# Optimization experiments

Measured on AMD Instinct MI355X. Metric: run time of the kernel, lower is better.

Reference implementation:

```python
import jax, jax.numpy as jnp
import numpy as np

N_NODES = 50000
N_EDGES = 800000
D_IN, D_HID, D_OUT = 128, 128, 64
BN_EPS = 1e-5


def gcn_conv(x, W, b, src, dst, ew, n):
    # PyG GCNConv: out[i] = sum_j norm_ij * (x @ W)[j] + b, with self-loops added
    xw = x @ W                                   # [N, D_out]
    loop = jnp.arange(n)
    s = jnp.concatenate([src, loop])             # add self-loops (weight 1)
    d = jnp.concatenate([dst, loop])
    w = jnp.concatenate([ew, jnp.ones((n,), x.dtype)])
    deg = jax.ops.segment_sum(w, d, num_segments=n)
    dinv = jnp.where(deg > 0, jax.lax.rsqrt(deg), 0.0)
    norm = dinv[s] * w * dinv[d]                 # symmetric normalization
    msg = xw[s] * norm[:, None]                  # gather + scale  [E+N, D_out]
    return jax.ops.segment_sum(msg, d, num_segments=n) + b


def setup_inputs() -> dict:
    key = jax.random.key(0)
    ks = jax.random.split(key, 12)
    x = jax.random.normal(ks[0], (N_NODES, D_IN), dtype=jnp.float32)
    edge_index = jax.random.randint(ks[1], (2, N_EDGES), 0, N_NODES, dtype=jnp.int64)
    edge_weight = jax.random.uniform(ks[2], (N_EDGES,), dtype=jnp.float32)
    W1 = jax.random.normal(ks[3], (D_IN, D_HID), dtype=jnp.float32) * 0.05
    b1 = jnp.zeros((D_HID,), jnp.float32)
    gamma = jnp.ones((D_HID,), jnp.float32)
    beta = jnp.zeros((D_HID,), jnp.float32)
    running_mean = jax.random.normal(ks[4], (D_HID,), dtype=jnp.float32) * 0.1
    running_var = jax.random.uniform(ks[5], (D_HID,), dtype=jnp.float32) + 0.5
    W2 = jax.random.normal(ks[6], (D_HID, D_OUT), dtype=jnp.float32) * 0.05
    b2 = jnp.zeros((D_OUT,), jnp.float32)
    return {"x": x, "edge_index": edge_index, "edge_weight": edge_weight,
            "W1": W1, "b1": b1, "gamma": gamma, "beta": beta,
            "running_mean": running_mean, "running_var": running_var,
            "W2": W2, "b2": b2}


def reference(x, edge_index, edge_weight, W1, b1, gamma, beta,
              running_mean, running_var, W2, b2):
    src, dst = edge_index[0], edge_index[1]
    n = x.shape[0]
    h = gcn_conv(x, W1, b1, src, dst, edge_weight, n)
    # BatchNorm1d in eval mode (running stats); dropout inactive in eval
    h = (h - running_mean) * jax.lax.rsqrt(running_var + BN_EPS) * gamma + beta
    h = jax.nn.relu(h)
    out = gcn_conv(h, W2, b2, src, dst, edge_weight, n)
    return out
```

## Files before the change

### kernel.cpp

```cpp
#include <hip/hip_runtime.h>
#include <hip/hip_fp16.h>

#define BN_EPS 1e-5f
#define PAD 64

typedef __attribute__((ext_vector_type(8))) short short8;
typedef __attribute__((ext_vector_type(4))) float f32x4;

static __device__ __forceinline__ unsigned short f2bf(float f) {
    unsigned u = __float_as_uint(f);
    u += 0x7FFF + ((u >> 16) & 1);
    return (unsigned short)(u >> 16);
}
static __device__ __forceinline__ float bf2f(unsigned short b) {
    return __uint_as_float((unsigned)b << 16);
}
static __device__ __forceinline__ unsigned pk(int s, float w) {
    return ((unsigned)s << 16) | (unsigned)__half_as_ushort(__float2half_rn(w));
}
static __device__ __forceinline__ float pw(unsigned e) {
    return __half2float(__ushort_as_half((unsigned short)(e & 0xFFFFu)));
}

__global__ __launch_bounds__(256) void k_fused(const int* __restrict__ src, const int* __restrict__ dst,
                                               const float* __restrict__ ew,
                                               int* cnt, unsigned* __restrict__ pad, int e, int gfill, int stride,
                                               const float* __restrict__ A, const float* __restrict__ W,
                                               unsigned short* __restrict__ C, int n,
                                               const float* __restrict__ b1, const float* __restrict__ gamma,
                                               const float* __restrict__ beta, const float* __restrict__ mean,
                                               const float* __restrict__ var,
                                               float* __restrict__ bnscale, float* __restrict__ bnshift,
                                               const float* __restrict__ W2, unsigned short* __restrict__ w2bf) {
    __shared__ unsigned short W1s[16384];
    int tid = threadIdx.x;
    int b = (int)blockIdx.x;
    int gGemm = (n + 63) / 64;

    bool isFill = ((b % stride) == 0) && (b / stride < gfill);
    if (isFill) {
        int i0 = ((b / stride) * 256 + tid) * 8;
        if (i0 + 7 < e) {
            int4   s0 = *(const int4*)(src + i0), s1 = *(const int4*)(src + i0 + 4);
            int4   d0 = *(const int4*)(dst + i0), d1 = *(const int4*)(dst + i0 + 4);
            float4 w0 = *(const float4*)(ew + i0), w1 = *(const float4*)(ew + i0 + 4);
            int p0 = atomicAdd(&cnt[d0.x], 1);
            int p1 = atomicAdd(&cnt[d0.y], 1);
            int p2 = atomicAdd(&cnt[d0.z], 1);
            int p3 = atomicAdd(&cnt[d0.w], 1);
            int p4 = atomicAdd(&cnt[d1.x], 1);
            int p5 = atomicAdd(&cnt[d1.y], 1);
            int p6 = atomicAdd(&cnt[d1.z], 1);
            int p7 = atomicAdd(&cnt[d1.w], 1);
            if (p0 < PAD) pad[(size_t)d0.x * PAD + p0] = pk(s0.x, w0.x);
            if (p1 < PAD) pad[(size_t)d0.y * PAD + p1] = pk(s0.y, w0.y);
            if (p2 < PAD) pad[(size_t)d0.z * PAD + p2] = pk(s0.z, w0.z);
            if (p3 < PAD) pad[(size_t)d0.w * PAD + p3] = pk(s0.w, w0.w);
            if (p4 < PAD) pad[(size_t)d1.x * PAD + p4] = pk(s1.x, w1.x);
            if (p5 < PAD) pad[(size_t)d1.y * PAD + p5] = pk(s1.y, w1.y);
            if (p6 < PAD) pad[(size_t)d1.z * PAD + p6] = pk(s1.z, w1.z);
            if (p7 < PAD) pad[(size_t)d1.w * PAD + p7] = pk(s1.w, w1.w);
        } else {
            for (int i = i0; i < e; ++i) {
                int d = dst[i];
                int p = atomicAdd(&cnt[d], 1);
                if (p < PAD) pad[(size_t)d * PAD + p] = pk(src[i], ew[i]);
            }
        }
        return;
    }

    int fillsBefore = (b == 0) ? 0 : min(gfill, (b - 1) / stride + 1);
    int g = b - fillsBefore;
    if (g == gGemm) {
        if (tid < 128) {
            float sc = gamma[tid] * rsqrtf(var[tid] + BN_EPS);
            bnscale[tid] = sc;
            bnshift[tid] = (b1[tid] - mean[tid]) * sc + beta[tid];
        }
        const float4* W4 = (const float4*)W2;
        ushort4* O = (ushort4*)w2bf;
        #pragma unroll
        for (int q = 0; q < 8; ++q) {
            float4 v = W4[q * 256 + tid];
            O[q * 256 + tid] = make_ushort4(f2bf(v.x), f2bf(v.y), f2bf(v.z), f2bf(v.w));
        }
        return;
    }

    int row0 = g * 64;

    {
        int k  = tid >> 1;
        int c0 = (tid & 1) * 64;
        int kk = k >> 5, lg = (k >> 3) & 3, ii = k & 7;
        int tbase = kk * 4096 + lg * 128 + ii;
        const float4* Wr = (const float4*)(W + (size_t)k * 128 + c0);
        #pragma unroll
        for (int j = 0; j < 16; ++j) {
            float4 v = Wr[j];
            int n0 = c0 + j * 4;
            W1s[tbase + ((n0 + 0) >> 4) * 512 + ((n0 + 0) & 15) * 8] = f2bf(v.x);
            W1s[tbase + ((n0 + 1) >> 4) * 512 + ((n0 + 1) & 15) * 8] = f2bf(v.y);
            W1s[tbase + ((n0 + 2) >> 4) * 512 + ((n0 + 2) & 15) * 8] = f2bf(v.z);
            W1s[tbase + ((n0 + 3) >> 4) * 512 + ((n0 + 3) & 15) * 8] = f2bf(v.w);
        }
    }
    __syncthreads();

    int w = tid >> 6, lane = tid & 63;
    int arow = row0 + w * 16 + (lane & 15);
    if (arow > n - 1) arow = n - 1;
    const float* xrow = A + (size_t)arow * 128 + ((lane >> 4) * 8);
    const unsigned short* Wl = W1s + (size_t)lane * 8;

    f32x4 z = {0.f, 0.f, 0.f, 0.f};
    f32x4 acc0 = z, acc1 = z, acc2 = z, acc3 = z, acc4 = z, acc5 = z, acc6 = z, acc7 = z;

    #pragma unroll
    for (int kk = 0; kk < 4; ++kk) {
        float4 v0 = *(const float4*)(xrow + kk * 32);
        float4 v1 = *(const float4*)(xrow + kk * 32 + 4);
        short8 a;
        a[0] = (short)f2bf(v0.x); a[1] = (short)f2bf(v0.y);
        a[2] = (short)f2bf(v0.z); a[3] = (short)f2bf(v0.w);
        a[4] = (short)f2bf(v1.x); a[5] = (short)f2bf(v1.y);
        a[6] = (short)f2bf(v1.z); a[7] = (short)f2bf(v1.w);
        const unsigned short* Wk = Wl + kk * 4096;
        short8 b0 = *(const short8*)(Wk);
        short8 b1 = *(const short8*)(Wk + 512);
        short8 b2 = *(const short8*)(Wk + 1024);
        short8 b3 = *(const short8*)(Wk + 1536);
        short8 b4 = *(const short8*)(Wk + 2048);
        short8 b5 = *(const short8*)(Wk + 2560);
        short8 b6 = *(const short8*)(Wk + 3072);
        short8 b7 = *(const short8*)(Wk + 3584);
        acc0 = __builtin_amdgcn_mfma_f32_16x16x32_bf16(a, b0, acc0, 0, 0, 0);
        acc1 = __builtin_amdgcn_mfma_f32_16x16x32_bf16(a, b1, acc1, 0, 0, 0);
        acc2 = __builtin_amdgcn_mfma_f32_16x16x32_bf16(a, b2, acc2, 0, 0, 0);
        acc3 = __builtin_amdgcn_mfma_f32_16x16x32_bf16(a, b3, acc3, 0, 0, 0);
        acc4 = __builtin_amdgcn_mfma_f32_16x16x32_bf16(a, b4, acc4, 0, 0, 0);
        acc5 = __builtin_amdgcn_mfma_f32_16x16x32_bf16(a, b5, acc5, 0, 0, 0);
        acc6 = __builtin_amdgcn_mfma_f32_16x16x32_bf16(a, b6, acc6, 0, 0, 0);
        acc7 = __builtin_amdgcn_mfma_f32_16x16x32_bf16(a, b7, acc7, 0, 0, 0);
    }

    int rw = row0 + w * 16 + ((lane >> 4) << 2);
    int cb = lane & 15;
    #define STORE_NT(av, nt)                                                              \
        if (rw + 0 < n) C[(size_t)(rw + 0) * 128 + (nt)*16 + cb] = f2bf(av[0]);           \
        if (rw + 1 < n) C[(size_t)(rw + 1) * 128 + (nt)*16 + cb] = f2bf(av[1]);           \
        if (rw + 2 < n) C[(size_t)(rw + 2) * 128 + (nt)*16 + cb] = f2bf(av[2]);           \
        if (rw + 3 < n) C[(size_t)(rw + 3) * 128 + (nt)*16 + cb] = f2bf(av[3]);
    STORE_NT(acc0, 0) STORE_NT(acc1, 1) STORE_NT(acc2, 2) STORE_NT(acc3, 3)
    STORE_NT(acc4, 4) STORE_NT(acc5, 5) STORE_NT(acc6, 6) STORE_NT(acc7, 7)
    #undef STORE_NT
}

__global__ __launch_bounds__(256) void k_deg(const int* __restrict__ cnt, const unsigned* __restrict__ pad,
                                             float* __restrict__ dinv, int n) {
    int i = blockIdx.x * 256 + threadIdx.x;
    if (i < n) {
        int c = min(cnt[i], PAD);
        size_t base = (size_t)i * PAD;
        const uint4* row = (const uint4*)(pad + base);
        float s = 1.0f;
        int p = 0;
        for (; p + 3 < c; p += 4) {
            uint4 v = row[p >> 2];
            s += pw(v.x) + pw(v.y) + pw(v.z) + pw(v.w);
        }
        for (; p < c; ++p) s += pw(pad[base + p]);
        dinv[i] = rsqrtf(s);
    }
}

__global__ __launch_bounds__(256) void k_ag12(const unsigned short* __restrict__ xw, const int* __restrict__ cnt,
                                              const unsigned* __restrict__ pad,
                                              const float* __restrict__ dinv,
                                              const float* __restrict__ scale, const float* __restrict__ shift,
                                              const unsigned short* __restrict__ w2bf,
                                              unsigned short* __restrict__ hw2, int n) {
    __shared__ unsigned short W2s[128 * 64];
    int tid = threadIdx.x;
    {
        const uint4* s4 = (const uint4*)w2bf;
        uint4* d4 = (uint4*)W2s;
        #pragma unroll
        for (int q = 0; q < 4; ++q) d4[q * 256 + tid] = s4[q * 256 + tid];
    }
    __syncthreads();

    int g = tid >> 5;
    int lc = tid & 31;
    int node = blockIdx.x * 8 + g;
    if (node >= n) return;

    unsigned hu0, hu1;
    {
        const ushort4* X4 = (const ushort4*)xw;
        float di = dinv[node];
        int c = min(cnt[node], PAD);
        size_t base = (size_t)node * PAD;
        ushort4 q0 = X4[(size_t)node * 32 + lc];
        float4 acc0 = make_float4(bf2f(q0.x) * di, bf2f(q0.y) * di, bf2f(q0.z) * di, bf2f(q0.w) * di);
        float4 acc1 = make_float4(0, 0, 0, 0);
        float4 acc2 = make_float4(0, 0, 0, 0);
        float4 acc3 = make_float4(0, 0, 0, 0);
        int p = 0;
        for (; p + 3 < c; p += 4) {
            uint4 ee = *(const uint4*)(pad + base + p);
            float w0 = pw(ee.x) * dinv[ee.x >> 16];
            float w1 = pw(ee.y) * dinv[ee.y >> 16];
            float w2 = pw(ee.z) * dinv[ee.z >> 16];
            float w3 = pw(ee.w) * dinv[ee.w >> 16];
            ushort4 a = X4[(size_t)(ee.x >> 16) * 32 + lc];
            ushort4 b = X4[(size_t)(ee.y >> 16) * 32 + lc];
            ushort4 gg = X4[(size_t)(ee.z >> 16) * 32 + lc];
            ushort4 d = X4[(size_t)(ee.w >> 16) * 32 + lc];
            acc0.x += w0 * bf2f(a.x); acc0.y += w0 * bf2f(a.y); acc0.z += w0 * bf2f(a.z); acc0.w += w0 * bf2f(a.w);
            acc1.x += w1 * bf2f(b.x); acc1.y += w1 * bf2f(b.y); acc1.z += w1 * bf2f(b.z); acc1.w += w1 * bf2f(b.w);
            acc2.x += w2 * bf2f(gg.x); acc2.y += w2 * bf2f(gg.y); acc2.z += w2 * bf2f(gg.z); acc2.w += w2 * bf2f(gg.w);
            acc3.x += w3 * bf2f(d.x); acc3.y += w3 * bf2f(d.y); acc3.z += w3 * bf2f(d.z); acc3.w += w3 * bf2f(d.w);
        }
        for (; p < c; ++p) {
            unsigned e0 = pad[base + p];
            float w0 = pw(e0) * dinv[e0 >> 16];
            ushort4 a = X4[(size_t)(e0 >> 16) * 32 + lc];
            acc0.x += w0 * bf2f(a.x); acc0.y += w0 * bf2f(a.y); acc0.z += w0 * bf2f(a.z); acc0.w += w0 * bf2f(a.w);
        }
        acc0.x = (acc0.x + acc1.x + acc2.x + acc3.x) * di;
        acc0.y = (acc0.y + acc1.y + acc2.y + acc3.y) * di;
        acc0.z = (acc0.z + acc1.z + acc2.z + acc3.z) * di;
        acc0.w = (acc0.w + acc1.w + acc2.w + acc3.w) * di;
        float4 Sc = ((const float4*)scale)[lc];
        float4 Sh = ((const float4*)shift)[lc];
        unsigned short r0 = f2bf(fmaxf(acc0.x * Sc.x + Sh.x, 0.0f));
        unsigned short r1 = f2bf(fmaxf(acc0.y * Sc.y + Sh.y, 0.0f));
        unsigned short r2 = f2bf(fmaxf(acc0.z * Sc.z + Sh.z, 0.0f));
        unsigned short r3 = f2bf(fmaxf(acc0.w * Sc.w + Sh.w, 0.0f));
        hu0 = ((unsigned)r1 << 16) | (unsigned)r0;
        hu1 = ((unsigned)r3 << 16) | (unsigned)r2;
    }

    float a0 = 0.0f, a1 = 0.0f;
    const unsigned* W2u = (const unsigned*)W2s;
    #pragma unroll 8
    for (int k = 0; k < 32; ++k) {
        unsigned p0 = (unsigned)__shfl((int)hu0, k, 32);
        unsigned p1 = (unsigned)__shfl((int)hu1, k, 32);
        float h0 = bf2f((unsigned short)(p0 & 0xFFFFu));
        float h1 = bf2f((unsigned short)(p0 >> 16));
        float h2 = bf2f((unsigned short)(p1 & 0xFFFFu));
        float h3 = bf2f((unsigned short)(p1 >> 16));
        unsigned w0u = W2u[(4 * k + 0) * 32 + lc];
        unsigned w1u = W2u[(4 * k + 1) * 32 + lc];
        unsigned w2u = W2u[(4 * k + 2) * 32 + lc];
        unsigned w3u = W2u[(4 * k + 3) * 32 + lc];
        a0 += h0 * bf2f((unsigned short)(w0u & 0xFFFFu));
        a1 += h0 * bf2f((unsigned short)(w0u >> 16));
        a0 += h1 * bf2f((unsigned short)(w1u & 0xFFFFu));
        a1 += h1 * bf2f((unsigned short)(w1u >> 16));
        a0 += h2 * bf2f((unsigned short)(w2u & 0xFFFFu));
        a1 += h2 * bf2f((unsigned short)(w2u >> 16));
        a0 += h3 * bf2f((unsigned short)(w3u & 0xFFFFu));
        a1 += h3 * bf2f((unsigned short)(w3u >> 16));
    }
    unsigned outp = ((unsigned)f2bf(a1) << 16) | (unsigned)f2bf(a0);
    ((unsigned*)hw2)[(size_t)node * 32 + lc] = outp;
}

__global__ __launch_bounds__(256) void k_agg2(const unsigned short* __restrict__ hw, const int* __restrict__ cnt,
                                              const unsigned* __restrict__ pad,
                                              const float* __restrict__ dinv,
                                              const float* __restrict__ b2, float* __restrict__ out, int n) {
    int node = blockIdx.x * 16 + (threadIdx.x >> 4);
    if (node >= n) return;
    int lc = threadIdx.x & 15;
    const ushort4* X4 = (const ushort4*)hw;
    float di = dinv[node];
    int c = min(cnt[node], PAD);
    size_t base = (size_t)node * PAD;
    ushort4 q0 = X4[(size_t)node * 16 + lc];
    float4 acc0 = make_float4(bf2f(q0.x) * di, bf2f(q0.y) * di, bf2f(q0.z) * di, bf2f(q0.w) * di);
    float4 acc1 = make_float4(0, 0, 0, 0);
    float4 acc2 = make_float4(0, 0, 0, 0);
    float4 acc3 = make_float4(0, 0, 0, 0);
    int p = 0;
    for (; p + 3 < c; p += 4) {
        uint4 ee = *(const uint4*)(pad + base + p);
        float w0 = pw(ee.x) * dinv[ee.x >> 16];
        float w1 = pw(ee.y) * dinv[ee.y >> 16];
        float w2 = pw(ee.z) * dinv[ee.z >> 16];
        float w3 = pw(ee.w) * dinv[ee.w >> 16];
        ushort4 a = X4[(size_t)(ee.x >> 16) * 16 + lc];
        ushort4 b = X4[(size_t)(ee.y >> 16) * 16 + lc];
        ushort4 g = X4[(size_t)(ee.z >> 16) * 16 + lc];
        ushort4 d = X4[(size_t)(ee.w >> 16) * 16 + lc];
        acc0.x += w0 * bf2f(a.x); acc0.y += w0 * bf2f(a.y); acc0.z += w0 * bf2f(a.z); acc0.w += w0 * bf2f(a.w);
        acc1.x += w1 * bf2f(b.x); acc1.y += w1 * bf2f(b.y); acc1.z += w1 * bf2f(b.z); acc1.w += w1 * bf2f(b.w);
        acc2.x += w2 * bf2f(g.x); acc2.y += w2 * bf2f(g.y); acc2.z += w2 * bf2f(g.z); acc2.w += w2 * bf2f(g.w);
        acc3.x += w3 * bf2f(d.x); acc3.y += w3 * bf2f(d.y); acc3.z += w3 * bf2f(d.z); acc3.w += w3 * bf2f(d.w);
    }
    for (; p < c; ++p) {
        unsigned e0 = pad[base + p];
        float w0 = pw(e0) * dinv[e0 >> 16];
        ushort4 a = X4[(size_t)(e0 >> 16) * 16 + lc];
        acc0.x += w0 * bf2f(a.x); acc0.y += w0 * bf2f(a.y); acc0.z += w0 * bf2f(a.z); acc0.w += w0 * bf2f(a.w);
    }
    float4 B = ((const float4*)b2)[lc];
    acc0.x = (acc0.x + acc1.x + acc2.x + acc3.x) * di + B.x;
    acc0.y = (acc0.y + acc1.y + acc2.y + acc3.y) * di + B.y;
    acc0.z = (acc0.z + acc1.z + acc2.z + acc3.z) * di + B.z;
    acc0.w = (acc0.w + acc1.w + acc2.w + acc3.w) * di + B.w;
    ((float4*)out)[(size_t)node * 16 + lc] = acc0;
}


extern "C" void kernel_launch(void* const* d_in, const int* in_sizes, int n_in,
                              void* d_out, int out_size, void* d_ws, size_t ws_size,
                              hipStream_t stream) {
    const float* x     = (const float*)d_in[0];
    const int*   ei    = (const int*)d_in[1];
    const float* ew    = (const float*)d_in[2];
    const float* W1    = (const float*)d_in[3];
    const float* b1    = (const float*)d_in[4];
    const float* gamma = (const float*)d_in[5];
    const float* beta  = (const float*)d_in[6];
    const float* rmean = (const float*)d_in[7];
    const float* rvar  = (const float*)d_in[8];
    const float* W2    = (const float*)d_in[9];
    const float* b2    = (const float*)d_in[10];
    float* out = (float*)d_out;

    int N = in_sizes[0] / 128;
    int E = in_sizes[2];
    const int* src = ei;
    const int* dst = ei + E;

    char* p = (char*)d_ws;
    auto carve = [&](size_t bytes) { char* q = p; p += (bytes + 255) & ~(size_t)255; return (void*)q; };
    int*      cnt     = (int*)     carve(sizeof(int) * (size_t)N);
    unsigned* pad     = (unsigned*)carve(sizeof(unsigned) * (size_t)N * PAD);
    float*    dinv    = (float*)   carve(sizeof(float) * (size_t)N);
    float*    bnscale = (float*)   carve(sizeof(float) * 128);
    float*    bnshift = (float*)   carve(sizeof(float) * 128);
    unsigned short* w2bf = (unsigned short*)carve(sizeof(unsigned short) * 128 * 64);
    unsigned short* xw1  = (unsigned short*)carve(sizeof(unsigned short) * (size_t)N * 128);
    unsigned short* hw2  = (unsigned short*)carve(sizeof(unsigned short) * (size_t)N * 64);

    int gN    = (N + 255) / 256;
    int gFill = (E + 2047) / 2048;
    int gGemm = (N + 63) / 64;
    int T     = gFill + gGemm + 1;
    int S     = T / gFill;
    if (S < 2) S = 2;

    hipMemsetAsync(cnt, 0, sizeof(int) * (size_t)N, stream);
    k_fused <<<T, 256, 0, stream>>>(src, dst, ew, cnt, pad, E, gFill, S,
                                    x, W1, xw1, N,
                                    b1, gamma, beta, rmean, rvar, bnscale, bnshift,
                                    W2, w2bf);
    k_deg   <<<gN, 256, 0, stream>>>(cnt, pad, dinv, N);
    k_ag12  <<<(N + 7) / 8, 256, 0, stream>>>(xw1, cnt, pad, dinv, bnscale, bnshift, w2bf, hw2, N);
    k_agg2  <<<(N + 15) / 16, 256, 0, stream>>>(hw2, cnt, pad, dinv, b2, out, N);
}
```

Baseline: 214.5 us.

## Build padded adjacency via two-level binning with block-local LDS counting

Replaces per-edge global atomics on per-node counters and scattered 4-byte writes with a two-phase bucket sort. Edges are first binned by destination block of 256 nodes using LDS atomics plus one global atomic per bin per block. A new kernel then builds each block's padded rows in shared memory, computes degrees, and writes the rows out coalesced. This aims to cut global atomic contention and random-write traffic, at the cost of an extra intermediate buffer and a fixed per-bin capacity (CAP) that silently drops edges if a bin overflows. The k_csr kernel also uses 64KB+ of shared memory, which limits occupancy.

```diff
diff --git a/kernel.cpp b/kernel.cpp
--- a/kernel.cpp
+++ b/kernel.cpp
@@ -3,6 +3,7 @@
 
 #define BN_EPS 1e-5f
 #define PAD 64
+#define CAP 4608
 
 typedef __attribute__((ext_vector_type(8))) short short8;
 typedef __attribute__((ext_vector_type(4))) float f32x4;
@@ -24,7 +25,8 @@
 
 __global__ __launch_bounds__(256) void k_fused(const int* __restrict__ src, const int* __restrict__ dst,
                                                const float* __restrict__ ew,
-                                               int* cnt, unsigned* __restrict__ pad, int e, int gfill, int stride,
+                                               uint2* __restrict__ bins, int* __restrict__ gcnt,
+                                               int e, int gfill, int stride, int nb,
                                                const float* __restrict__ A, const float* __restrict__ W,
                                                unsigned short* __restrict__ C, int n,
                                                const float* __restrict__ b1, const float* __restrict__ gamma,
@@ -39,33 +41,49 @@
 
     bool isFill = ((b % stride) == 0) && (b / stride < gfill);
     if (isFill) {
+        int* lcnt  = (int*)W1s;
+        int* gbase = lcnt + 256;
+        lcnt[tid] = 0;
+        __syncthreads();
+
         int i0 = ((b / stride) * 256 + tid) * 8;
+        unsigned pv[8];  int bk[8]; int rk[8]; unsigned dl[8];
+        int cnt8 = 0;
         if (i0 + 7 < e) {
             int4   s0 = *(const int4*)(src + i0), s1 = *(const int4*)(src + i0 + 4);
             int4   d0 = *(const int4*)(dst + i0), d1 = *(const int4*)(dst + i0 + 4);
             float4 w0 = *(const float4*)(ew + i0), w1 = *(const float4*)(ew + i0 + 4);
-            int p0 = atomicAdd(&cnt[d0.x], 1);
-            int p1 = atomicAdd(&cnt[d0.y], 1);
-            int p2 = atomicAdd(&cnt[d0.z], 1);
-            int p3 = atomicAdd(&cnt[d0.w], 1);
-            int p4 = atomicAdd(&cnt[d1.x], 1);
-            int p5 = atomicAdd(&cnt[d1.y], 1);
-            int p6 = atomicAdd(&cnt[d1.z], 1);
-            int p7 = atomicAdd(&cnt[d1.w], 1);
-            if (p0 < PAD) pad[(size_t)d0.x * PAD + p0] = pk(s0.x, w0.x);
-            if (p1 < PAD) pad[(size_t)d0.y * PAD + p1] = pk(s0.y, w0.y);
-            if (p2 < PAD) pad[(size_t)d0.z * PAD + p2] = pk(s0.z, w0.z);
-            if (p3 < PAD) pad[(size_t)d0.w * PAD + p3] = pk(s0.w, w0.w);
-            if (p4 < PAD) pad[(size_t)d1.x * PAD + p4] = pk(s1.x, w1.x);
-            if (p5 < PAD) pad[(size_t)d1.y * PAD + p5] = pk(s1.y, w1.y);
-            if (p6 < PAD) pad[(size_t)d1.z * PAD + p6] = pk(s1.z, w1.z);
-            if (p7 < PAD) pad[(size_t)d1.w * PAD + p7] = pk(s1.w, w1.w);
+            int   ss[8] = {s0.x, s0.y, s0.z, s0.w, s1.x, s1.y, s1.z, s1.w};
+            int   dd[8] = {d0.x, d0.y, d0.z, d0.w, d1.x, d1.y, d1.z, d1.w};
+            float ww[8] = {w0.x, w0.y, w0.z, w0.w, w1.x, w1.y, w1.z, w1.w};
+            #pragma unroll
+            for (int j = 0; j < 8; ++j) {
+                int d_ = dd[j];
+                bk[j] = d_ >> 8;
+                dl[j] = (unsigned)(d_ & 255);
+                rk[j] = atomicAdd(&lcnt[bk[j]], 1);
+                pv[j] = pk(ss[j], ww[j]);
+            }
+            cnt8 = 8;
         } else {
-            for (int i = i0; i < e; ++i) {
-                int d = dst[i];
-                int p = atomicAdd(&cnt[d], 1);
-                if (p < PAD) pad[(size_t)d * PAD + p] = pk(src[i], ew[i]);
+            for (int j = 0; j < 8; ++j) {
+                int i = i0 + j;
+                if (i < e) {
+                    int d_ = dst[i];
+                    bk[j] = d_ >> 8;
+                    dl[j] = (unsigned)(d_ & 255);
+                    rk[j] = atomicAdd(&lcnt[bk[j]], 1);
+                    pv[j] = pk(src[i], ew[i]);
+                    cnt8 = j + 1;
+                }
             }
+        }
+        __syncthreads();
+        if (tid < nb) gbase[tid] = atomicAdd(&gcnt[tid], lcnt[tid]);
+        __syncthreads();
+        for (int j = 0; j < cnt8; ++j) {
+            int pos = gbase[bk[j]] + rk[j];
+            if (pos < CAP) bins[(size_t)bk[j] * CAP + pos] = make_uint2(pv[j], dl[j]);
         }
         return;
     }
@@ -157,22 +175,40 @@
     #undef STORE_NT
 }
 
-__global__ __launch_bounds__(256) void k_deg(const int* __restrict__ cnt, const unsigned* __restrict__ pad,
+__global__ __launch_bounds__(256) void k_csr(const uint2* __restrict__ bins, const int* __restrict__ gcnt,
+                                             unsigned* __restrict__ pad, int* __restrict__ cnt,
                                              float* __restrict__ dinv, int n) {
-    int i = blockIdx.x * 256 + threadIdx.x;
-    if (i < n) {
-        int c = min(cnt[i], PAD);
-        size_t base = (size_t)i * PAD;
-        const uint4* row = (const uint4*)(pad + base);
+    __shared__ unsigned csr[256 * PAD];
+    __shared__ int lc[256];
+    int tid = threadIdx.x;
+    int b = (int)blockIdx.x;
+    int node0 = b << 8;
+    int nodes = min(256, n - node0);
+    lc[tid] = 0;
+    __syncthreads();
+
+    int m = gcnt[b];
+    if (m > CAP) m = CAP;
+    const uint2* seg = bins + (size_t)b * CAP;
+    for (int i = tid; i < m; i += 256) {
+        uint2 v = seg[i];
+        int r = atomicAdd(&lc[v.y], 1);
+        if (r < PAD) csr[v.y * PAD + r] = v.x;
+    }
+    __syncthreads();
+
+    if (tid < nodes) {
+        int c = lc[tid];
+        cnt[node0 + tid] = c;
+        int cc = min(c, PAD);
         float s = 1.0f;
-        int p = 0;
-        for (; p + 3 < c; p += 4) {
-            uint4 v = row[p >> 2];
-            s += pw(v.x) + pw(v.y) + pw(v.z) + pw(v.w);
-        }
-        for (; p < c; ++p) s += pw(pad[base + p]);
-        dinv[i] = rsqrtf(s);
-    }
+        for (int p = 0; p < cc; ++p) s += pw(csr[tid * PAD + p]);
+        dinv[node0 + tid] = rsqrtf(s);
+    }
+    const uint4* s4 = (const uint4*)csr;
+    uint4* d4 = (uint4*)(pad + (size_t)node0 * PAD);
+    int tot = nodes * (PAD / 4);
+    for (int q = tid; q < tot; q += 256) d4[q] = s4[q];
 }
 
 __global__ __launch_bounds__(256) void k_ag12(const unsigned short* __restrict__ xw, const int* __restrict__ cnt,
@@ -337,6 +373,7 @@
     int E = in_sizes[2];
     const int* src = ei;
     const int* dst = ei + E;
+    int NB = (N + 255) >> 8;
 
     char* p = (char*)d_ws;
     auto carve = [&](size_t bytes) { char* q = p; p += (bytes + 255) & ~(size_t)255; return (void*)q; };
@@ -348,20 +385,21 @@
     unsigned short* w2bf = (unsigned short*)carve(sizeof(unsigned short) * 128 * 64);
     unsigned short* xw1  = (unsigned short*)carve(sizeof(unsigned short) * (size_t)N * 128);
     unsigned short* hw2  = (unsigned short*)carve(sizeof(unsigned short) * (size_t)N * 64);
-
-    int gN    = (N + 255) / 256;
+    int*      gcnt    = (int*)     carve(sizeof(int) * (size_t)NB);
+    uint2*    bins    = (uint2*)   carve(sizeof(uint2) * (size_t)NB * CAP);
+
     int gFill = (E + 2047) / 2048;
     int gGemm = (N + 63) / 64;
     int T     = gFill + gGemm + 1;
     int S     = T / gFill;
     if (S < 2) S = 2;
 
-    hipMemsetAsync(cnt, 0, sizeof(int) * (size_t)N, stream);
-    k_fused <<<T, 256, 0, stream>>>(src, dst, ew, cnt, pad, E, gFill, S,
+    hipMemsetAsync(gcnt, 0, sizeof(int) * (size_t)NB, stream);
+    k_fused <<<T, 256, 0, stream>>>(src, dst, ew, bins, gcnt, E, gFill, S, NB,
                                     x, W1, xw1, N,
                                     b1, gamma, beta, rmean, rvar, bnscale, bnshift,
                                     W2, w2bf);
-    k_deg   <<<gN, 256, 0, stream>>>(cnt, pad, dinv, N);
+    k_csr   <<<NB, 256, 0, stream>>>(bins, gcnt, pad, cnt, dinv, N);
     k_ag12  <<<(N + 7) / 8, 256, 0, stream>>>(xw1, cnt, pad, dinv, bnscale, bnshift, w2bf, hw2, N);
     k_agg2  <<<(N + 15) / 16, 256, 0, stream>>>(hw2, cnt, pad, dinv, b2, out, N);
 }
```

Result: faster. 193.0 us (-10.0%).
